# Kernel tuning notes

Hardware: AMD Instinct MI355X
Metric: run time of the kernel (lower is better)

Reference implementation:

```python
import jax, jax.numpy as jnp
import numpy as np

N, IN_DIM, HID, HEADS, HOPS, NCLS, E = 20000, 1536, 256, 4, 3, 3, 320000
HD = HID // HEADS
EPS = 1e-5
NEG_SLOPE = 0.2


def layer_norm(x, g, b):
    mu = jnp.mean(x, axis=-1, keepdims=True)
    var = jnp.var(x, axis=-1, keepdims=True)
    return (x - mu) * jax.lax.rsqrt(var + EPS) * g + b


def gatv2(x, src, dst, Wl, bl, Wr, br, att, bias):
    # x: [N, HID]; src/dst: [E'] (self loops included)
    xl = (x @ Wl + bl).reshape(N, HEADS, HD)  # source transform
    xr = (x @ Wr + br).reshape(N, HEADS, HD)  # target transform
    e = jax.nn.leaky_relu(xl[src] + xr[dst], NEG_SLOPE)          # [E', H, D]
    logits = jnp.einsum('ehd,hd->eh', e, att)                     # [E', H]
    m = jax.ops.segment_max(logits, dst, num_segments=N)         # [N, H]
    ex = jnp.exp(logits - m[dst])
    denom = jax.ops.segment_sum(ex, dst, num_segments=N)
    alpha = ex / denom[dst]                                       # softmax per dst
    msg = xl[src] * alpha[:, :, None]                             # [E', H, D]
    out = jax.ops.segment_sum(msg, dst, num_segments=N)
    return out.reshape(N, HID) + bias


def setup_inputs() -> dict:
    key = jax.random.key(0)
    ks = jax.random.split(key, 20)
    s = lambda k, shp, sc: jax.random.normal(k, shp, jnp.float32) * sc
    return {
        'features': s(ks[0], (N, IN_DIM), 1.0),
        'edge_index': jax.random.randint(ks[1], (2, E), 0, N, jnp.int64),
        'proj_W': s(ks[2], (IN_DIM, HID), 0.02),
        'proj_b': jnp.zeros((HID,), jnp.float32),
        'n0_g': jnp.ones((HID,), jnp.float32),
        'n0_b': jnp.zeros((HID,), jnp.float32),
        'Wl': s(ks[3], (HOPS, HID, HID), 0.05),
        'bl': jnp.zeros((HOPS, HID), jnp.float32),
        'Wr': s(ks[4], (HOPS, HID, HID), 0.05),
        'br': jnp.zeros((HOPS, HID), jnp.float32),
        'att': s(ks[5], (HOPS, HEADS, HD), 0.1),
        'gbias': jnp.zeros((HOPS, HID), jnp.float32),
        'ln_g': jnp.ones((HOPS, HID), jnp.float32),
        'ln_b': jnp.zeros((HOPS, HID), jnp.float32),
        'h1_W': s(ks[6], (HID, HID), 0.05),
        'h1_b': jnp.zeros((HID,), jnp.float32),
        'h2_W': s(ks[7], (HID, NCLS), 0.05),
        'h2_b': jnp.zeros((NCLS,), jnp.float32),
    }


def reference(features, edge_index, proj_W, proj_b, n0_g, n0_b, Wl, bl, Wr, br,
              att, gbias, ln_g, ln_b, h1_W, h1_b, h2_W, h2_b):
    # add self loops (PyG GATv2Conv default)
    loop = jnp.arange(N, dtype=edge_index.dtype)
    src = jnp.concatenate([edge_index[0], loop])
    dst = jnp.concatenate([edge_index[1], loop])

    x = layer_norm(features @ proj_W + proj_b, n0_g, n0_b)
    for h in range(HOPS):
        g = gatv2(x, src, dst, Wl[h], bl[h], Wr[h], br[h], att[h], gbias[h])
        x = layer_norm(g + x, ln_g[h], ln_b[h])
    # head (dropout inactive at eval); torch GELU is exact erf form
    x = jax.nn.gelu(x @ h1_W + h1_b, approximate=False)
    return x @ h2_W + h2_b
```

## Files before the change

### kernel.cpp

```cpp
#include <hip/hip_runtime.h>
#include <hip/hip_bf16.h>
#include <math.h>

#define NN 20000
#define INDIM 1536
#define HID 256
#define NE 320000
#define NEDGE (NE + NN)
#define EPSV 1e-5f
#define NEG 0.2f

typedef unsigned short ushort_b;
typedef unsigned int uint32;
typedef __bf16 bf16x8 __attribute__((ext_vector_type(8)));
typedef float f32x4 __attribute__((ext_vector_type(4)));

#define AS1(p) ((const __attribute__((address_space(1))) void*)(p))
#define AS3(p) ((__attribute__((address_space(3))) void*)(p))

__device__ inline ushort_b f2bf(float x) {
  union { float f; uint32 u; } v; v.f = x;
  uint32 r = v.u + 0x7FFFu + ((v.u >> 16) & 1u);
  return (ushort_b)(r >> 16);
}
__device__ inline float bf2f(ushort_b h) {
  union { uint32 u; float f; } v; v.u = ((uint32)h) << 16;
  return v.f;
}
__device__ inline float u2f(uint32 u) {
  union { uint32 u; float f; } v; v.u = u; return v.f;
}
__device__ inline uint32 cvtpk_bf16(float a, float b) {
  uint32 r;
  asm("v_cvt_pk_bf16_f32 %0, %1, %2" : "=v"(r) : "v"(a), "v"(b));
  return r;
}
__device__ inline float4 ldbf4(const ushort_b* p) {
  ushort4 u = *(const ushort4*)p;
  float4 f;
  f.x = bf2f(u.x); f.y = bf2f(u.y); f.z = bf2f(u.z); f.w = bf2f(u.w);
  return f;
}
__device__ inline float4 us4f(ushort4 u) {
  float4 f;
  f.x = bf2f(u.x); f.y = bf2f(u.y); f.z = bf2f(u.z); f.w = bf2f(u.w);
  return f;
}

template<int OUTMODE, int DUALB>
__global__ __launch_bounds__(256, 3) void gemm_mfma(
    const float* __restrict__ Af,
    const ushort_b* __restrict__ Bt0, const ushort_b* __restrict__ Bt1,
    const float* __restrict__ bias0, const float* __restrict__ bias1,
    void* __restrict__ C0, void* __restrict__ C1,
    int Mstore, int Kloop, int Kstride)
{
  __shared__ ushort_b Bs[3 * 8192];
  const ushort_b* Bt;
  const float* bias;
  void* Cv;
  int kbase;
  if (DUALB) {
    Bt = blockIdx.z ? Bt1 : Bt0;
    bias = blockIdx.z ? bias1 : bias0;
    Cv = blockIdx.z ? C1 : C0;
    kbase = 0;
  } else {
    Bt = Bt0;
    bias = blockIdx.z ? bias1 : bias0;
    Cv = (float*)C0 + (size_t)blockIdx.z * NN * HID;
    kbase = blockIdx.z * Kloop;
  }

  int tid = threadIdx.x;
  int wave = tid >> 6, lane = tid & 63;
  int quad = lane >> 4, mrow = lane & 15;
  int r0 = blockIdx.y * 128;
  int p  = blockIdx.x;
  int nk = Kloop >> 5;
  int nchunk = Kstride >> 5;
  int cb = kbase >> 5;

  int arow0 = r0 + (wave << 5) + mrow;
  int arow1 = arow0 + 16;
  if (arow0 >= Mstore) arow0 = Mstore - 1;
  if (arow1 >= Mstore) arow1 = Mstore - 1;
  const float* Aptr0 = Af + (size_t)arow0 * Kstride + kbase + (quad << 3);
  const float* Aptr1 = Af + (size_t)arow1 * Kstride + kbase + (quad << 3);

  f32x4 acc[2][8] = {};
  float pA0[16], pA1[16];

  auto issueB = [&](int kc, int buf) {
    const char* g = (const char*)Bt + (((size_t)(p * nchunk + (cb + kc))) << 14);
    char* l = (char*)Bs + buf * 16384;
    int o = tid << 4;
#pragma unroll
    for (int pl = 0; pl < 2; pl++) {
      int off = (pl << 13) + o;
      __builtin_amdgcn_global_load_lds(AS1(g + off), AS3(l + off), 16, 0, 0);
      __builtin_amdgcn_global_load_lds(AS1(g + off + 4096), AS3(l + off + 4096), 16, 0, 0);
    }
  };
  auto loadA = [&](int k, float* dst) {
    const float* s0 = Aptr0 + (k << 5);
    const float* s1 = Aptr1 + (k << 5);
    *(float4*)(dst)      = *(const float4*)(s0);
    *(float4*)(dst + 4)  = *(const float4*)(s0 + 4);
    *(float4*)(dst + 8)  = *(const float4*)(s1);
    *(float4*)(dst + 12) = *(const float4*)(s1 + 4);
  };
  auto cvtFrag = [&](const float* s, bf16x8& hh, bf16x8& ll) {
    union { bf16x8 v; uint32 u[4]; } H, L;
#pragma unroll
    for (int q2 = 0; q2 < 4; q2++) {
      float a = s[2 * q2], b = s[2 * q2 + 1];
      uint32 hp = cvtpk_bf16(a, b);
      float fa = u2f(hp << 16);
      float fb = u2f(hp & 0xffff0000u);
      H.u[q2] = hp;
      L.u[q2] = cvtpk_bf16(a - fa, b - fb);
    }
    hh = H.v; ll = L.v;
  };
  auto computeStage = [&](int buf, const bf16x8& ah0, const bf16x8& al0,
                          const bf16x8& ah1, const bf16x8& al1) {
    const ushort_b* bp = Bs + buf * 8192;
#pragma unroll
    for (int u = 0; u < 8; u++) {
      bf16x8 bh = *(const bf16x8*)(bp + (u << 9) + (lane << 3));
      bf16x8 bl = *(const bf16x8*)(bp + 4096 + (u << 9) + (lane << 3));
      acc[0][u] = __builtin_amdgcn_mfma_f32_16x16x32_bf16(ah0, bh, acc[0][u], 0, 0, 0);
      acc[0][u] = __builtin_amdgcn_mfma_f32_16x16x32_bf16(al0, bh, acc[0][u], 0, 0, 0);
      acc[0][u] = __builtin_amdgcn_mfma_f32_16x16x32_bf16(ah0, bl, acc[0][u], 0, 0, 0);
      acc[1][u] = __builtin_amdgcn_mfma_f32_16x16x32_bf16(ah1, bh, acc[1][u], 0, 0, 0);
      acc[1][u] = __builtin_amdgcn_mfma_f32_16x16x32_bf16(al1, bh, acc[1][u], 0, 0, 0);
      acc[1][u] = __builtin_amdgcn_mfma_f32_16x16x32_bf16(ah1, bl, acc[1][u], 0, 0, 0);
    }
  };

  loadA(0, pA0);
  issueB(0, 0);
  issueB(1, 1);
  loadA(1, pA1);
  asm volatile("s_waitcnt vmcnt(8)" ::: "memory");
  __builtin_amdgcn_sched_barrier(0);
  __builtin_amdgcn_s_barrier();
  __builtin_amdgcn_sched_barrier(0);

  int bcur = 0;
  for (int k = 0; k < nk; k += 2) {
    int b1 = bcur + 1; if (b1 >= 3) b1 -= 3;
    int b2 = bcur + 2; if (b2 >= 3) b2 -= 3;

    {
      bf16x8 ah0, al0, ah1, al1;
      cvtFrag(pA0, ah0, al0);
      cvtFrag(pA0 + 8, ah1, al1);
      if (k + 2 < nk) { issueB(k + 2, b2); loadA(k + 2, pA0); }
      computeStage(bcur, ah0, al0, ah1, al1);
      if (k + 2 < nk) { asm volatile("s_waitcnt vmcnt(8)" ::: "memory"); }
      else            { asm volatile("s_waitcnt vmcnt(4)" ::: "memory"); }
      __builtin_amdgcn_sched_barrier(0);
      __builtin_amdgcn_s_barrier();
      __builtin_amdgcn_sched_barrier(0);
    }
    {
      bf16x8 ah0, al0, ah1, al1;
      cvtFrag(pA1, ah0, al0);
      cvtFrag(pA1 + 8, ah1, al1);
      if (k + 3 < nk) { issueB(k + 3, bcur); loadA(k + 3, pA1); }
      computeStage(b1, ah0, al0, ah1, al1);
      if (k + 3 < nk) {
        asm volatile("s_waitcnt vmcnt(8)" ::: "memory");
        __builtin_amdgcn_sched_barrier(0);
        __builtin_amdgcn_s_barrier();
        __builtin_amdgcn_sched_barrier(0);
      }
    }
    bcur = b2;
  }

#pragma unroll
  for (int u = 0; u < 8; u++) {
    int col = (p << 7) + (u << 4) + mrow;
    float bb = bias[col];
#pragma unroll
    for (int t = 0; t < 2; t++) {
#pragma unroll
      for (int r = 0; r < 4; r++) {
        int row = r0 + (wave << 5) + (t << 4) + (quad << 2) + r;
        if (row < Mstore) {
          float v = acc[t][u][r] + bb;
          if (OUTMODE == 3) v = 0.5f * v * (1.f + erff(v * 0.70710678118654752f));
          if (OUTMODE == 2) ((ushort_b*)Cv)[(size_t)row * 256 + col] = f2bf(v);
          else              ((float*)Cv)[(size_t)row * 256 + col] = v;
        }
      }
    }
  }
}

__device__ inline void prep_body(const float* __restrict__ W, int ldw, int nchunk,
                                 ushort_b* __restrict__ out, int c, int p, int tid)
{
  ushort_b* base = out + (((size_t)(p * nchunk + c)) << 13);
#pragma unroll
  for (int g0 = 0; g0 < 2; g0++) {
    int g = tid + (g0 << 8);
    int u = g >> 6, l = g & 63;
    int quad = l >> 4, mrow = l & 15;
    int col = (p << 7) + (u << 4) + mrow;
    int krow = (c << 5) + (quad << 3);
    uint32 hu[4], lu[4];
#pragma unroll
    for (int q2 = 0; q2 < 4; q2++) {
      float a = W[(size_t)(krow + 2 * q2) * ldw + col];
      float b = W[(size_t)(krow + 2 * q2 + 1) * ldw + col];
      ushort_b h0 = f2bf(a), h1 = f2bf(b);
      hu[q2] = (uint32)h0 | ((uint32)h1 << 16);
      lu[q2] = (uint32)f2bf(a - bf2f(h0)) | ((uint32)f2bf(b - bf2f(h1)) << 16);
    }
    *(uint4*)(base + (size_t)g * 8)        = make_uint4(hu[0], hu[1], hu[2], hu[3]);
    *(uint4*)(base + 4096 + (size_t)g * 8) = make_uint4(lu[0], lu[1], lu[2], lu[3]);
  }
}

__global__ __launch_bounds__(256) void prep_all(
    const float* __restrict__ projW, const float* __restrict__ Wl,
    const float* __restrict__ Wr, const float* __restrict__ h1W,
    ushort_b* __restrict__ wtp, ushort_b* __restrict__ w7,
    int* __restrict__ cnt)
{
  int z = blockIdx.z, c = blockIdx.x, p = blockIdx.y;
  if (z == 7) {
    int lin = (c * 2 + p) * 256 + threadIdx.x;
    if (lin < NN) cnt[lin] = 0;
    prep_body(projW, HID, INDIM / 32, wtp, c, p, threadIdx.x);
  } else {
    if (c >= 8) return;
    const float* W = (z < 3) ? Wl + (size_t)z * 65536
                   : (z < 6) ? Wr + (size_t)(z - 3) * 65536
                             : h1W;
    prep_body(W, 256, 8, w7 + (size_t)z * 131072, c, p, threadIdx.x);
  }
}

__global__ __launch_bounds__(256) void ln_sum_kernel(
    const float* __restrict__ in,
    const float* __restrict__ g, const float* __restrict__ b,
    float* __restrict__ out, int n)
{
  int wave = threadIdx.x >> 6, lane = threadIdx.x & 63;
  int row = blockIdx.x * 4 + wave;
  if (row >= n) return;
  int c = lane << 2;
  const float* p0 = in + (size_t)row * HID + c;
  float4 v  = *(const float4*)(p0);
  float4 v1 = *(const float4*)(p0 + (size_t)NN * HID);
  v.x += v1.x; v.y += v1.y; v.z += v1.z; v.w += v1.w;
  float s1 = v.x + v.y + v.z + v.w;
  float s2 = v.x * v.x + v.y * v.y + v.z * v.z + v.w * v.w;
#pragma unroll
  for (int m = 1; m < 64; m <<= 1) {
    s1 += __shfl_xor(s1, m, 64);
    s2 += __shfl_xor(s2, m, 64);
  }
  float mu = s1 * (1.f / 256.f);
  float var = s2 * (1.f / 256.f) - mu * mu;
  float rstd = rsqrtf(var + EPSV);
  float4 gv = *(const float4*)(g + c);
  float4 bv = *(const float4*)(b + c);
  float4 o;
  o.x = (v.x - mu) * rstd * gv.x + bv.x;
  o.y = (v.y - mu) * rstd * gv.y + bv.y;
  o.z = (v.z - mu) * rstd * gv.z + bv.z;
  o.w = (v.w - mu) * rstd * gv.w + bv.w;
  *(float4*)(out + (size_t)row * HID + c) = o;
}

__global__ void count_kernel(const int* __restrict__ ei, int* __restrict__ cnt,
                             float* __restrict__ zbias)
{
  int e = blockIdx.x * blockDim.x + threadIdx.x;
  if (e < HID) zbias[e] = 0.f;
  if (e < NEDGE) {
    int d = (e < NE) ? ei[NE + e] : (e - NE);
    atomicAdd(&cnt[d], 1);
  }
}

__global__ __launch_bounds__(1024) void scan_kernel(
    const int* __restrict__ cnt, int* __restrict__ offs, int* __restrict__ cursor)
{
  __shared__ int sums[1024];
  int tid = threadIdx.x;
  const int CH = 20;
  int base = tid * CH;
  int loc[CH];
  int s = 0;
#pragma unroll
  for (int i = 0; i < CH; i++) {
    int idx = base + i;
    int v = (idx < NN) ? cnt[idx] : 0;
    loc[i] = s;
    s += v;
  }
  sums[tid] = s;
  __syncthreads();
  for (int off = 1; off < 1024; off <<= 1) {
    int t = (tid >= off) ? sums[tid - off] : 0;
    __syncthreads();
    sums[tid] += t;
    __syncthreads();
  }
  int pre = (tid == 0) ? 0 : sums[tid - 1];
#pragma unroll
  for (int i = 0; i < CH; i++) {
    int idx = base + i;
    if (idx < NN) { int e = pre + loc[i]; offs[idx] = e; cursor[idx] = e; }
  }
  if (tid == 0) offs[NN] = NEDGE;
}

__global__ void scatter_kernel(const int* __restrict__ ei, int* __restrict__ cursor,
                               int* __restrict__ csr_src)
{
  int e = blockIdx.x * blockDim.x + threadIdx.x;
  if (e < NEDGE) {
    int s, d;
    if (e < NE) { s = ei[e]; d = ei[NE + e]; }
    else { s = e - NE; d = e - NE; }
    int p = atomicAdd(&cursor[d], 1);
    csr_src[p] = s;
  }
}

__device__ inline float edge_logit(float4 xv, float4 xrv, float4 attv) {
  float e0 = xv.x + xrv.x, e1 = xv.y + xrv.y, e2 = xv.z + xrv.z, e3 = xv.w + xrv.w;
  e0 = (e0 > 0.f) ? e0 : NEG * e0;
  e1 = (e1 > 0.f) ? e1 : NEG * e1;
  e2 = (e2 > 0.f) ? e2 : NEG * e2;
  e3 = (e3 > 0.f) ? e3 : NEG * e3;
  float lc = e0 * attv.x + e1 * attv.y + e2 * attv.z + e3 * attv.w;
  lc += __shfl_xor(lc, 1, 16);
  lc += __shfl_xor(lc, 2, 16);
  lc += __shfl_xor(lc, 4, 16);
  lc += __shfl_xor(lc, 8, 16);
  return lc;
}

#define ACCUM(i, wt, xv) {                             \
    lS[i] += wt;                                       \
    pS##i##0 += wt * xv.x; pS##i##1 += wt * xv.y;      \
    pS##i##2 += wt * xv.z; pS##i##3 += wt * xv.w; }

__global__ __launch_bounds__(256, 6) void gat_kernel(
    const ushort_b* __restrict__ xl, const ushort_b* __restrict__ xr,
    const float* __restrict__ x_in, const float* __restrict__ att,
    const float* __restrict__ gbias, const float* __restrict__ ln_g,
    const float* __restrict__ ln_b, const int* __restrict__ offs,
    const int* __restrict__ csr_src, float* __restrict__ x_out)
{
  int wave = threadIdx.x >> 6, lane = threadIdx.x & 63;
  int node = blockIdx.x * 4 + wave;
  int c = lane << 2;
  float4 xrv = ldbf4(xr + (size_t)node * HID + c);
  float4 attv = *(const float4*)(att + c);

  float lS[4] = {0.f, 0.f, 0.f, 0.f};
  float pS00 = 0.f, pS01 = 0.f, pS02 = 0.f, pS03 = 0.f;
  float pS10 = 0.f, pS11 = 0.f, pS12 = 0.f, pS13 = 0.f;
  float pS20 = 0.f, pS21 = 0.f, pS22 = 0.f, pS23 = 0.f;
  float pS30 = 0.f, pS31 = 0.f, pS32 = 0.f, pS33 = 0.f;

  int e = offs[node], end = offs[node + 1];
  int last = end - 1;
#define CI(x) ((x) <= last ? (x) : last)
  auto G = [&](int i) { return *(const ushort4*)(xl + (size_t)i * HID + c); };

  int i0 = csr_src[e], i1 = csr_src[CI(e + 1)];
  int i2 = csr_src[CI(e + 2)], i3 = csr_src[CI(e + 3)];
  ushort4 a0 = G(i0), a1 = G(i1), a2 = G(i2), a3 = G(i3);
  int en = e + 4;
  bool more = en < end;
  int j0, j1, j2, j3;
  if (more) {
    j0 = csr_src[en]; j1 = csr_src[CI(en + 1)];
    j2 = csr_src[CI(en + 2)]; j3 = csr_src[CI(en + 3)];
  }

  for (;;) {
    int rem = end - e;
    int en2 = en + 4;
    bool more2 = more && (en2 < end);
    ushort4 b0, b1, b2, b3;
    if (more) {
      b0 = G(j0); b1 = G(j1); b2 = G(j2); b3 = G(j3);
      if (more2) {
        j0 = csr_src[en2]; j1 = csr_src[CI(en2 + 1)];
        j2 = csr_src[CI(en2 + 2)]; j3 = csr_src[CI(en2 + 3)];
      }
    }
    float4 x0v = us4f(a0);
    float4 x1v = us4f(a1);
    float4 x2v = us4f(a2);
    float4 x3v = us4f(a3);
    float g0 = edge_logit(x0v, xrv, attv);
    float g1 = edge_logit(x1v, xrv, attv);
    float g2 = edge_logit(x2v, xrv, attv);
    float g3 = edge_logit(x3v, xrv, attv);
    float w0 = __expf(g0);
    float w1 = (rem > 1) ? __expf(g1) : 0.f;
    float w2 = (rem > 2) ? __expf(g2) : 0.f;
    float w3 = (rem > 3) ? __expf(g3) : 0.f;
    ACCUM(0, w0, x0v);
    ACCUM(1, w1, x1v);
    ACCUM(2, w2, x2v);
    ACCUM(3, w3, x3v);
    if (!more) break;
    e = en; en = en2; more = more2;
    a0 = b0; a1 = b1; a2 = b2; a3 = b3;
  }
#undef CI

  float l  = lS[0] + lS[1] + lS[2] + lS[3];
  float q0 = pS00 + pS10 + pS20 + pS30;
  float q1 = pS01 + pS11 + pS21 + pS31;
  float q2 = pS02 + pS12 + pS22 + pS32;
  float q3 = pS03 + pS13 + pS23 + pS33;

  float inv = 1.f / l;
  float4 xv = *(const float4*)(x_in + (size_t)node * HID + c);
  float4 gb = *(const float4*)(gbias + c);
  float o0 = q0 * inv + gb.x + xv.x;
  float o1 = q1 * inv + gb.y + xv.y;
  float o2 = q2 * inv + gb.z + xv.z;
  float o3 = q3 * inv + gb.w + xv.w;
  float s1s = o0 + o1 + o2 + o3;
  float s2s = o0 * o0 + o1 * o1 + o2 * o2 + o3 * o3;
#pragma unroll
  for (int mmk = 1; mmk < 64; mmk <<= 1) {
    s1s += __shfl_xor(s1s, mmk, 64);
    s2s += __shfl_xor(s2s, mmk, 64);
  }
  float mu = s1s * (1.f / 256.f);
  float var = s2s * (1.f / 256.f) - mu * mu;
  float rstd = rsqrtf(var + EPSV);
  float4 gv = *(const float4*)(ln_g + c);
  float4 bv = *(const float4*)(ln_b + c);
  float4 o;
  o.x = (o0 - mu) * rstd * gv.x + bv.x;
  o.y = (o1 - mu) * rstd * gv.y + bv.y;
  o.z = (o2 - mu) * rstd * gv.z + bv.z;
  o.w = (o3 - mu) * rstd * gv.w + bv.w;
  *(float4*)(x_out + (size_t)node * HID + c) = o;
}

__global__ __launch_bounds__(256) void head2_kernel(
    const float* __restrict__ t1, const float* __restrict__ W,
    const float* __restrict__ bias, float* __restrict__ out)
{
  int wave = threadIdx.x >> 6, lane = threadIdx.x & 63;
  int row = blockIdx.x * 4 + wave;
  if (row >= NN) return;
  int c = lane << 2;
  float4 v = *(const float4*)(t1 + (size_t)row * HID + c);
  float p0 = 0.f, p1 = 0.f, p2 = 0.f;
#pragma unroll
  for (int j = 0; j < 4; j++) {
    float vj = (&v.x)[j];
    p0 += vj * W[(c + j) * 3 + 0];
    p1 += vj * W[(c + j) * 3 + 1];
    p2 += vj * W[(c + j) * 3 + 2];
  }
#pragma unroll
  for (int mm = 1; mm < 64; mm <<= 1) {
    p0 += __shfl_xor(p0, mm, 64);
    p1 += __shfl_xor(p1, mm, 64);
    p2 += __shfl_xor(p2, mm, 64);
  }
  if (lane == 0) {
    out[(size_t)row * 3 + 0] = p0 + bias[0];
    out[(size_t)row * 3 + 1] = p1 + bias[1];
    out[(size_t)row * 3 + 2] = p2 + bias[2];
  }
}

extern "C" void kernel_launch(void* const* d_in, const int* in_sizes, int n_in,
                              void* d_out, int out_size, void* d_ws, size_t ws_size,
                              hipStream_t stream)
{
  const float* features = (const float*)d_in[0];
  const int*   ei       = (const int*)d_in[1];
  const float* proj_W   = (const float*)d_in[2];
  const float* proj_b   = (const float*)d_in[3];
  const float* n0_g     = (const float*)d_in[4];
  const float* n0_b     = (const float*)d_in[5];
  const float* Wl       = (const float*)d_in[6];
  const float* bl       = (const float*)d_in[7];
  const float* Wr       = (const float*)d_in[8];
  const float* br       = (const float*)d_in[9];
  const float* att      = (const float*)d_in[10];
  const float* gbias    = (const float*)d_in[11];
  const float* ln_g     = (const float*)d_in[12];
  const float* ln_b     = (const float*)d_in[13];
  const float* h1_W     = (const float*)d_in[14];
  const float* h1_b     = (const float*)d_in[15];
  const float* h2_W     = (const float*)d_in[16];
  const float* h2_b     = (const float*)d_in[17];
  float* out = (float*)d_out;

  char* w = (char*)d_ws;
  float*    x0    = (float*)w;    w += (size_t)NN * HID * 4;
  float*    x1    = (float*)w;    w += (size_t)NN * HID * 4;
  float*    part1 = (float*)w;    w += (size_t)NN * HID * 4;
  ushort_b* xlb   = (ushort_b*)w; w += (size_t)NN * HID * 2;
  ushort_b* xrb   = (ushort_b*)w; w += (size_t)NN * HID * 2;
  ushort_b* wtp   = (ushort_b*)w; w += (size_t)2 * HID * INDIM * 2;
  ushort_b* w7    = (ushort_b*)w; w += (size_t)14 * HID * HID * 2;
  float* zbias = (float*)w; w += (size_t)HID * 4;
  int* cnt     = (int*)w;  w += (size_t)NN * 4;
  int* offs    = (int*)w;  w += (size_t)(NN + 1) * 4;
  int* cursor  = (int*)w;  w += (size_t)NN * 4;
  int* csr     = (int*)w;  w += (size_t)NEDGE * 4;

  prep_all<<<dim3(INDIM / 32, 2, 8), 256, 0, stream>>>(proj_W, Wl, Wr, h1_W, wtp, w7, cnt);
  count_kernel<<<(NEDGE + 255) / 256, 256, 0, stream>>>(ei, cnt, zbias);
  scan_kernel<<<1, 1024, 0, stream>>>(cnt, offs, cursor);
  scatter_kernel<<<(NEDGE + 255) / 256, 256, 0, stream>>>(ei, cursor, csr);

  const int MB = (NN + 127) / 128;
  dim3 gproj(2, MB, 2);
  dim3 ghop(2, MB, 2);
  dim3 gsingle(2, MB, 1);

  gemm_mfma<0, 0><<<gproj, 256, 0, stream>>>(
      features, wtp, wtp, proj_b, zbias, x0, x0, NN, INDIM / 2, INDIM);
  ln_sum_kernel<<<(NN + 3) / 4, 256, 0, stream>>>(x0, n0_g, n0_b, x0, NN);

  float* xcur = x0;
  float* xnxt = x1;
  for (int h = 0; h < 3; h++) {
    gemm_mfma<2, 1><<<ghop, 256, 0, stream>>>(
        xcur, w7 + (size_t)h * 131072, w7 + (size_t)(3 + h) * 131072,
        bl + h * HID, br + h * HID, xlb, xrb, NN, HID, HID);
    gat_kernel<<<NN / 4, 256, 0, stream>>>(
        xlb, xrb, xcur, att + h * HID, gbias + h * HID,
        ln_g + h * HID, ln_b + h * HID, offs, csr, xnxt);
    float* t = xcur; xcur = xnxt; xnxt = t;
  }

  gemm_mfma<3, 1><<<gsingle, 256, 0, stream>>>(
      xcur, w7 + (size_t)6 * 131072, w7 + (size_t)6 * 131072,
      h1_b, h1_b, part1, part1, NN, HID, HID);
  head2_kernel<<<(NN + 3) / 4, 256, 0, stream>>>(part1, h2_W, h2_b, out);
}
```

Baseline: 578.0 us.

## Add full-K resident-B GEMM with 64-column tiles for hop and head GEMMs

Adds a gemm_fullB kernel for the K=256 hop and head GEMMs. It loads the whole 64-column B slice for all K chunks into LDS up front, then runs the eight K steps without per-stage barriers or a triple-buffer rotation. Each block computes 64 instead of 128 output columns, which doubles the grid in x to raise parallelism for these small GEMMs. The cost is more A re-reads across column blocks and 64KB of LDS per block, which limits occupancy to about two blocks per CU.

```diff
diff --git a/kernel.cpp b/kernel.cpp
--- a/kernel.cpp
+++ b/kernel.cpp
@@ -45,6 +45,19 @@
   float4 f;
   f.x = bf2f(u.x); f.y = bf2f(u.y); f.z = bf2f(u.z); f.w = bf2f(u.w);
   return f;
+}
+__device__ inline void cvtFragP(const float* s, bf16x8& hh, bf16x8& ll) {
+  union { bf16x8 v; uint32 u[4]; } H, L;
+#pragma unroll
+  for (int q2 = 0; q2 < 4; q2++) {
+    float a = s[2 * q2], b = s[2 * q2 + 1];
+    uint32 hp = cvtpk_bf16(a, b);
+    float fa = u2f(hp << 16);
+    float fb = u2f(hp & 0xffff0000u);
+    H.u[q2] = hp;
+    L.u[q2] = cvtpk_bf16(a - fa, b - fb);
+  }
+  hh = H.v; ll = L.v;
 }
 
 template<int OUTMODE, int DUALB>
@@ -110,19 +123,6 @@
     *(float4*)(dst + 8)  = *(const float4*)(s1);
     *(float4*)(dst + 12) = *(const float4*)(s1 + 4);
   };
-  auto cvtFrag = [&](const float* s, bf16x8& hh, bf16x8& ll) {
-    union { bf16x8 v; uint32 u[4]; } H, L;
-#pragma unroll
-    for (int q2 = 0; q2 < 4; q2++) {
-      float a = s[2 * q2], b = s[2 * q2 + 1];
-      uint32 hp = cvtpk_bf16(a, b);
-      float fa = u2f(hp << 16);
-      float fb = u2f(hp & 0xffff0000u);
-      H.u[q2] = hp;
-      L.u[q2] = cvtpk_bf16(a - fa, b - fb);
-    }
-    hh = H.v; ll = L.v;
-  };
   auto computeStage = [&](int buf, const bf16x8& ah0, const bf16x8& al0,
                           const bf16x8& ah1, const bf16x8& al1) {
     const ushort_b* bp = Bs + buf * 8192;
@@ -155,8 +155,8 @@
 
     {
       bf16x8 ah0, al0, ah1, al1;
-      cvtFrag(pA0, ah0, al0);
-      cvtFrag(pA0 + 8, ah1, al1);
+      cvtFragP(pA0, ah0, al0);
+      cvtFragP(pA0 + 8, ah1, al1);
       if (k + 2 < nk) { issueB(k + 2, b2); loadA(k + 2, pA0); }
       computeStage(bcur, ah0, al0, ah1, al1);
       if (k + 2 < nk) { asm volatile("s_waitcnt vmcnt(8)" ::: "memory"); }
@@ -167,8 +167,8 @@
     }
     {
       bf16x8 ah0, al0, ah1, al1;
-      cvtFrag(pA1, ah0, al0);
-      cvtFrag(pA1 + 8, ah1, al1);
+      cvtFragP(pA1, ah0, al0);
+      cvtFragP(pA1 + 8, ah1, al1);
       if (k + 3 < nk) { issueB(k + 3, bcur); loadA(k + 3, pA1); }
       computeStage(b1, ah0, al0, ah1, al1);
       if (k + 3 < nk) {
@@ -184,6 +184,99 @@
 #pragma unroll
   for (int u = 0; u < 8; u++) {
     int col = (p << 7) + (u << 4) + mrow;
+    float bb = bias[col];
+#pragma unroll
+    for (int t = 0; t < 2; t++) {
+#pragma unroll
+      for (int r = 0; r < 4; r++) {
+        int row = r0 + (wave << 5) + (t << 4) + (quad << 2) + r;
+        if (row < Mstore) {
+          float v = acc[t][u][r] + bb;
+          if (OUTMODE == 3) v = 0.5f * v * (1.f + erff(v * 0.70710678118654752f));
+          if (OUTMODE == 2) ((ushort_b*)Cv)[(size_t)row * 256 + col] = f2bf(v);
+          else              ((float*)Cv)[(size_t)row * 256 + col] = v;
+        }
+      }
+    }
+  }
+}
+
+template<int OUTMODE>
+__global__ __launch_bounds__(256, 2) void gemm_fullB(
+    const float* __restrict__ Af,
+    const ushort_b* __restrict__ Bt0, const ushort_b* __restrict__ Bt1,
+    const float* __restrict__ bias0, const float* __restrict__ bias1,
+    void* __restrict__ C0, void* __restrict__ C1, int Mstore)
+{
+  __shared__ ushort_b Bs[32768];
+  const ushort_b* Bt = blockIdx.z ? Bt1 : Bt0;
+  const float* bias  = blockIdx.z ? bias1 : bias0;
+  void* Cv           = blockIdx.z ? C1 : C0;
+
+  int tid = threadIdx.x;
+  int wave = tid >> 6, lane = tid & 63;
+  int quad = lane >> 4, mrow = lane & 15;
+  int r0 = blockIdx.y * 128;
+  int p  = blockIdx.x;
+  int p128 = p >> 1, half = p & 1;
+
+  int arow0 = r0 + (wave << 5) + mrow;
+  int arow1 = arow0 + 16;
+  if (arow0 >= Mstore) arow0 = Mstore - 1;
+  if (arow1 >= Mstore) arow1 = Mstore - 1;
+  const float* Aptr0 = Af + (size_t)arow0 * HID + (quad << 3);
+  const float* Aptr1 = Af + (size_t)arow1 * HID + (quad << 3);
+
+  f32x4 acc[2][4] = {};
+  float pA0[16], pA1[16];
+
+  auto loadA = [&](int k, float* dst) {
+    const float* s0 = Aptr0 + (k << 5);
+    const float* s1 = Aptr1 + (k << 5);
+    *(float4*)(dst)      = *(const float4*)(s0);
+    *(float4*)(dst + 4)  = *(const float4*)(s0 + 4);
+    *(float4*)(dst + 8)  = *(const float4*)(s1);
+    *(float4*)(dst + 12) = *(const float4*)(s1 + 4);
+  };
+
+#pragma unroll
+  for (int c = 0; c < 8; c++) {
+#pragma unroll
+    for (int pl = 0; pl < 2; pl++) {
+      const char* g = (const char*)(Bt + ((size_t)(p128 * 8 + c) << 13)
+                                    + (pl << 12) + (half << 11)) + (tid << 4);
+      char* l = (char*)(Bs + (c << 12) + (pl << 11)) + (tid << 4);
+      __builtin_amdgcn_global_load_lds(AS1(g), AS3(l), 16, 0, 0);
+    }
+  }
+  loadA(0, pA0);
+  loadA(1, pA1);
+  __syncthreads();
+
+#pragma unroll
+  for (int k = 0; k < 8; k++) {
+    float* cur = (k & 1) ? pA1 : pA0;
+    bf16x8 ah0, al0, ah1, al1;
+    cvtFragP(cur, ah0, al0);
+    cvtFragP(cur + 8, ah1, al1);
+    if (k + 2 < 8) loadA(k + 2, cur);
+    const ushort_b* bp = Bs + (k << 12);
+#pragma unroll
+    for (int u = 0; u < 4; u++) {
+      bf16x8 bh = *(const bf16x8*)(bp + (u << 9) + (lane << 3));
+      bf16x8 bl = *(const bf16x8*)(bp + 2048 + (u << 9) + (lane << 3));
+      acc[0][u] = __builtin_amdgcn_mfma_f32_16x16x32_bf16(ah0, bh, acc[0][u], 0, 0, 0);
+      acc[0][u] = __builtin_amdgcn_mfma_f32_16x16x32_bf16(al0, bh, acc[0][u], 0, 0, 0);
+      acc[0][u] = __builtin_amdgcn_mfma_f32_16x16x32_bf16(ah0, bl, acc[0][u], 0, 0, 0);
+      acc[1][u] = __builtin_amdgcn_mfma_f32_16x16x32_bf16(ah1, bh, acc[1][u], 0, 0, 0);
+      acc[1][u] = __builtin_amdgcn_mfma_f32_16x16x32_bf16(al1, bh, acc[1][u], 0, 0, 0);
+      acc[1][u] = __builtin_amdgcn_mfma_f32_16x16x32_bf16(ah1, bl, acc[1][u], 0, 0, 0);
+    }
+  }
+
+#pragma unroll
+  for (int u = 0; u < 4; u++) {
+    int col = (p << 6) + (u << 4) + mrow;
     float bb = bias[col];
 #pragma unroll
     for (int t = 0; t < 2; t++) {
@@ -532,8 +625,8 @@
 
   const int MB = (NN + 127) / 128;
   dim3 gproj(2, MB, 2);
-  dim3 ghop(2, MB, 2);
-  dim3 gsingle(2, MB, 1);
+  dim3 ghop(4, MB, 2);
+  dim3 gh1(4, MB, 1);
 
   gemm_mfma<0, 0><<<gproj, 256, 0, stream>>>(
       features, wtp, wtp, proj_b, zbias, x0, x0, NN, INDIM / 2, INDIM);
@@ -542,17 +635,17 @@
   float* xcur = x0;
   float* xnxt = x1;
   for (int h = 0; h < 3; h++) {
-    gemm_mfma<2, 1><<<ghop, 256, 0, stream>>>(
+    gemm_fullB<2><<<ghop, 256, 0, stream>>>(
         xcur, w7 + (size_t)h * 131072, w7 + (size_t)(3 + h) * 131072,
-        bl + h * HID, br + h * HID, xlb, xrb, NN, HID, HID);
+        bl + h * HID, br + h * HID, xlb, xrb, NN);
     gat_kernel<<<NN / 4, 256, 0, stream>>>(
         xlb, xrb, xcur, att + h * HID, gbias + h * HID,
         ln_g + h * HID, ln_b + h * HID, offs, csr, xnxt);
     float* t = xcur; xcur = xnxt; xnxt = t;
   }
 
-  gemm_mfma<3, 1><<<gsingle, 256, 0, stream>>>(
+  gemm_fullB<3><<<gh1, 256, 0, stream>>>(
       xcur, w7 + (size_t)6 * 131072, w7 + (size_t)6 * 131072,
-      h1_b, h1_b, part1, part1, NN, HID, HID);
+      h1_b, h1_b, part1, part1, NN);
   head2_kernel<<<(NN + 3) / 4, 256, 0, stream>>>(part1, h2_W, h2_b, out);
 }
```

Result: slower. 618.6 us (+7.0%).
